# Kernel optimization log

Hardware: AMD Instinct MI355X
Metric: run time of the kernel (lower is better)

The kernel has to match this reference:

```python
import jax, jax.numpy as jnp
import numpy as np


def setup_inputs() -> dict:
    key = jax.random.key(0)
    ks = jax.random.split(key, 6)
    B, S, D_IN, D_OUT, E, R = 4, 2048, 4096, 4096, 8, 16
    x = jax.random.normal(ks[0], (B, S, D_IN), dtype=jnp.float32)
    probs = jax.random.uniform(ks[1], (B, E), dtype=jnp.float32)
    router_probs = probs / jnp.sum(probs, axis=-1, keepdims=True)
    weight = jax.random.normal(ks[2], (D_OUT, D_IN), dtype=jnp.float32) * 0.02
    bias = jax.random.normal(ks[3], (D_OUT,), dtype=jnp.float32) * 0.02
    lora_A = jax.random.normal(ks[4], (E, R, D_IN), dtype=jnp.float32) * 0.02
    lora_B = jax.random.normal(ks[5], (E, D_OUT, R), dtype=jnp.float32) * 0.02
    return {"x": x, "router_probs": router_probs, "weight": weight,
            "bias": bias, "lora_A": lora_A, "lora_B": lora_B}


def reference(x, router_probs, weight, bias, lora_A, lora_B):
    scaling = 2.0
    # base linear: [b,s,i] @ [o,i]^T + bias
    base_out = jnp.einsum('bsi,oi->bso', x, weight) + bias
    # low-rank per-expert projection: [b,s,e,r] (small: r=16)
    mid = jnp.einsum('bsi,eri->bser', x, lora_A)
    # weight by router probs (per batch, per expert) before up-projection
    mid_w = mid * router_probs[:, None, :, None]
    # sum over experts fused into the up-projection contraction
    delta = jnp.einsum('bser,eor->bso', mid_w, lora_B) * scaling
    return base_out + delta
```

## Files before the change

### kernel.cpp

```cpp
#include <hip/hip_runtime.h>


typedef _Float16 half8 __attribute__((ext_vector_type(8)));
typedef _Float16 half4 __attribute__((ext_vector_type(4)));
typedef float    f32x4 __attribute__((ext_vector_type(4)));

#define M_TOT 8192
#define N_TOT 4096
#define K_IN  4096
#define KA    4224
#define NT    132

__device__ __forceinline__ void cvt_store4(_Float16* p, float4 f) {
  half4 h;
  h[0] = (_Float16)f.x; h[1] = (_Float16)f.y;
  h[2] = (_Float16)f.z; h[3] = (_Float16)f.w;
  *(half4*)p = h;
}

template <int LOG2C, int DCOLS>
__global__ __launch_bounds__(256) void convert_f32_f16_t(
    const float* __restrict__ src, _Float16* __restrict__ dst, int total8) {
  for (int i = blockIdx.x * 256 + threadIdx.x; i < total8;
       i += gridDim.x * 256) {
    int base = i << 3;
    int r = base >> LOG2C;
    int c = base & ((1 << LOG2C) - 1);
    const float4* s = (const float4*)(src + (size_t)base);
    float4 f0 = s[0], f1 = s[1];
    half8 h;
    h[0]=(_Float16)f0.x; h[1]=(_Float16)f0.y; h[2]=(_Float16)f0.z; h[3]=(_Float16)f0.w;
    h[4]=(_Float16)f1.x; h[5]=(_Float16)f1.y; h[6]=(_Float16)f1.z; h[7]=(_Float16)f1.w;
    *(half8*)(dst + (size_t)r * DCOLS + c) = h;
  }
}

__global__ __launch_bounds__(256) void wtail_gather_f16(
    const float* __restrict__ loraB, _Float16* __restrict__ Wa) {
  int idx = blockIdx.x * 256 + threadIdx.x;
  int n = idx >> 7, j = idx & 127;
  int e = j >> 4, r = j & 15;
  Wa[(size_t)n * KA + K_IN + j] =
      (_Float16)loraB[((size_t)e * N_TOT + n) * 16 + r];
}

__global__ __launch_bounds__(256) void lorabf_gather_f32(
    const float* __restrict__ loraB, float* __restrict__ lorabf) {
  int idx = blockIdx.x * 256 + threadIdx.x;
  int n = idx >> 7, j = idx & 127;
  int e = j >> 4, r = j & 15;
  lorabf[(size_t)n * 128 + j] = loraB[((size_t)e * N_TOT + n) * 16 + r];
}

__global__ __launch_bounds__(256) void mid2_kernel(
    _Float16* __restrict__ Xa, const _Float16* __restrict__ lAh,
    const float* __restrict__ router) {
  __shared__ _Float16 As[32 * 64];
  __shared__ _Float16 Bs[128 * 64];
  int tid = threadIdx.x, lane = tid & 63, w = tid >> 6;
  int m0 = blockIdx.x * 32;
  int b = m0 >> 11;
  f32x4 acc[2][2] = {};

  for (int ks = 0; ks < 64; ++ks) {
    int kb = ks * 128;
    {
      const char* s = (const char*)Xa +
          (size_t)(m0 + w * 8 + (lane >> 3)) * (KA * 2) + kb + (lane & 7) * 16;
      __builtin_amdgcn_global_load_lds(
          (const __attribute__((address_space(1))) void*)s,
          (__attribute__((address_space(3))) void*)((char*)As + w * 1024), 16, 0, 0);
    }
#pragma unroll
    for (int i = 0; i < 4; ++i) {
      const char* s = (const char*)lAh +
          (size_t)((w * 4 + i) * 8 + (lane >> 3)) * (4096 * 2) + kb + (lane & 7) * 16;
      __builtin_amdgcn_global_load_lds(
          (const __attribute__((address_space(1))) void*)s,
          (__attribute__((address_space(3))) void*)((char*)Bs + (w * 4 + i) * 1024), 16, 0, 0);
    }
    __syncthreads();
#pragma unroll
    for (int kk = 0; kk < 2; ++kk) {
      half8 a[2], bf[2];
#pragma unroll
      for (int mi = 0; mi < 2; ++mi)
        a[mi] = *(const half8*)(As + (mi * 16 + (lane & 15)) * 64 + kk * 32 + (lane >> 4) * 8);
#pragma unroll
      for (int ni = 0; ni < 2; ++ni)
        bf[ni] = *(const half8*)(Bs + (w * 32 + ni * 16 + (lane & 15)) * 64 + kk * 32 + (lane >> 4) * 8);
#pragma unroll
      for (int mi = 0; mi < 2; ++mi)
#pragma unroll
        for (int ni = 0; ni < 2; ++ni)
          acc[mi][ni] = __builtin_amdgcn_mfma_f32_16x16x32_f16(a[mi], bf[ni], acc[mi][ni], 0, 0, 0);
    }
    __syncthreads();
  }

#pragma unroll
  for (int ni = 0; ni < 2; ++ni) {
    int j = w * 32 + ni * 16 + (lane & 15);
    int e = j >> 4;
    float sc = 2.0f * router[b * 8 + e];
#pragma unroll
    for (int mi = 0; mi < 2; ++mi) {
      f32x4 v = acc[mi][ni];
#pragma unroll
      for (int jj = 0; jj < 4; ++jj) {
        int m = m0 + mi * 16 + (lane >> 4) * 4 + jj;
        Xa[(size_t)m * KA + K_IN + j] = (_Float16)(v[jj] * sc);
      }
    }
  }
}

__global__ __launch_bounds__(256) void mid_kernel(
    const float* __restrict__ x, const float* __restrict__ loraA,
    const float* __restrict__ router, float* __restrict__ midw) {
  __shared__ _Float16 As[32 * 64];
  __shared__ _Float16 Bs[128 * 64];
  int tid = threadIdx.x, lane = tid & 63, w = tid >> 6;
  int m0 = blockIdx.x * 32;
  int b = m0 >> 11;
  f32x4 acc[2][2] = {};
  for (int ks = 0; ks < 64; ++ks) {
    int k0 = ks * 64;
#pragma unroll
    for (int it = 0; it < 2; ++it) {
      int idx = tid + it * 256;
      int r = idx >> 4, c4 = idx & 15;
      float4 f = *(const float4*)(x + (size_t)(m0 + r) * K_IN + k0 + c4 * 4);
      cvt_store4(As + r * 64 + c4 * 4, f);
    }
#pragma unroll
    for (int it = 0; it < 8; ++it) {
      int idx = tid + it * 256;
      int r = idx >> 4, c4 = idx & 15;
      float4 f = *(const float4*)(loraA + (size_t)r * K_IN + k0 + c4 * 4);
      cvt_store4(Bs + r * 64 + c4 * 4, f);
    }
    __syncthreads();
#pragma unroll
    for (int kk = 0; kk < 2; ++kk) {
      half8 a[2], bf[2];
#pragma unroll
      for (int mi = 0; mi < 2; ++mi)
        a[mi] = *(const half8*)(As + (mi * 16 + (lane & 15)) * 64 + kk * 32 + (lane >> 4) * 8);
#pragma unroll
      for (int ni = 0; ni < 2; ++ni)
        bf[ni] = *(const half8*)(Bs + (w * 32 + ni * 16 + (lane & 15)) * 64 + kk * 32 + (lane >> 4) * 8);
#pragma unroll
      for (int mi = 0; mi < 2; ++mi)
#pragma unroll
        for (int ni = 0; ni < 2; ++ni)
          acc[mi][ni] = __builtin_amdgcn_mfma_f32_16x16x32_f16(a[mi], bf[ni], acc[mi][ni], 0, 0, 0);
    }
    __syncthreads();
  }
#pragma unroll
  for (int ni = 0; ni < 2; ++ni) {
    int j = w * 32 + ni * 16 + (lane & 15);
    int e = j >> 4;
    float sc = 2.0f * router[b * 8 + e];
#pragma unroll
    for (int mi = 0; mi < 2; ++mi) {
      f32x4 v = acc[mi][ni];
#pragma unroll
      for (int jj = 0; jj < 4; ++jj) {
        int m = m0 + mi * 16 + (lane >> 4) * 4 + jj;
        midw[(size_t)m * 128 + j] = v[jj] * sc;
      }
    }
  }
}

#define BAR    __builtin_amdgcn_s_barrier()
#define SCHED0 __builtin_amdgcn_sched_barrier(0)
#define PRIO1  __builtin_amdgcn_s_setprio(1)
#define PRIO0  __builtin_amdgcn_s_setprio(0)
#define LGKM0  do { asm volatile("s_waitcnt lgkmcnt(0)" ::: "memory"); \
                    __builtin_amdgcn_sched_barrier(0); } while (0)
#define VMW8   asm volatile("s_waitcnt vmcnt(8)" ::: "memory")
#define VMW4   asm volatile("s_waitcnt vmcnt(4)" ::: "memory")
#define VMW0   asm volatile("s_waitcnt vmcnt(0)" ::: "memory")
#define GLOAD(src, dst) __builtin_amdgcn_global_load_lds( \
    (const __attribute__((address_space(1))) void*)(src), \
    (__attribute__((address_space(3))) void*)(dst), 16, 0, 0)

#define READS(SL) do { \
  _Pragma("unroll") for (int mi = 0; mi < 8; ++mi) \
    aF[mi] = *(const half8*)(LDS + (SL) * 16384 + \
                             (wm + mi * 16 + ln15) * 64 + rslot); \
  _Pragma("unroll") for (int ni = 0; ni < 4; ++ni) \
    bF[ni] = *(const half8*)(LDS + 65536 + (SL) * 16384 + \
                             (wn + ni * 16 + ln15) * 64 + rslot); \
  } while (0)

#define STAGE4(TT, SL) do { \
  const char* sA_ = XpC + (size_t)(TT) * 64; \
  const char* sB_ = WpC + (size_t)(TT) * 64; \
  GLOAD(sA_ + goff0, LDS + (SL) * 16384 + l0); \
  GLOAD(sA_ + goff1, LDS + (SL) * 16384 + l1); \
  GLOAD(sB_ + goff0, LDS + 65536 + (SL) * 16384 + l0); \
  GLOAD(sB_ + goff1, LDS + 65536 + (SL) * 16384 + l1); \
  } while (0)

#define MFMA32 do { \
  PRIO1; \
  _Pragma("unroll") for (int mi = 0; mi < 8; ++mi) \
    _Pragma("unroll") for (int ni = 0; ni < 4; ++ni) \
      acc[mi][ni] = __builtin_amdgcn_mfma_f32_16x16x32_f16( \
          aF[mi], bF[ni], acc[mi][ni], 0, 0, 0); \
  PRIO0; \
  } while (0)

#define TILE_FULL(SL) do { \
  READS(SL); \
  STAGE4(t4 + (SL) + 3, ((SL) + 3) & 3); \
  LGKM0; MFMA32; VMW8; BAR; SCHED0; \
  } while (0)

__global__ __launch_bounds__(512, 2) void gemm256(
    const _Float16* __restrict__ Xa, const _Float16* __restrict__ Wa,
    const float* __restrict__ bias, float* __restrict__ out) {
  __shared__ __align__(16) char LDS[131072];

  int tid = threadIdx.x, lane = tid & 63, w = tid >> 6;
  int ln15 = lane & 15, ln4 = lane >> 4;
  int wm = (w >> 2) * 128, wn = (w & 3) * 64;

  int bid = blockIdx.x;
  int xcd = bid & 7, idx = bid >> 3;
  int mt = (xcd & 3) * 8 + (idx & 7);
  int nt = (xcd >> 2) * 8 + (idx >> 3);
  int m0 = mt << 8, n0 = nt << 8;

  const char* XpC = (const char*)Xa + (size_t)m0 * (KA * 2);
  const char* WpC = (const char*)Wa + (size_t)n0 * (KA * 2);

  int i0 = tid, i1 = tid + 512;
  int goff0 = (i0 >> 2) * (KA * 2) + (((i0 & 3) ^ ((i0 >> 3) & 3)) * 16);
  int goff1 = (i1 >> 2) * (KA * 2) + (((i1 & 3) ^ ((i1 >> 3) & 3)) * 16);
  int l0 = i0 * 16, l1 = i1 * 16;

  int rslot = ((ln4 ^ ((lane >> 1) & 3)) * 16);

  f32x4 acc[8][4] = {};
  half8 aF[8], bF[4];

  STAGE4(0, 0); STAGE4(1, 1); STAGE4(2, 2);
  VMW8; BAR; SCHED0;

#pragma unroll 1
  for (int t4 = 0; t4 < NT - 4; t4 += 4) {
    TILE_FULL(0); TILE_FULL(1); TILE_FULL(2); TILE_FULL(3);
  }

  { READS(0); STAGE4(131, 3); LGKM0; MFMA32; VMW8; BAR; SCHED0; }
  { READS(1); LGKM0; MFMA32; VMW4; BAR; SCHED0; }
  { READS(2); LGKM0; MFMA32; VMW0; BAR; SCHED0; }
  { READS(3); LGKM0; MFMA32; }

#pragma unroll
  for (int ni = 0; ni < 4; ++ni) {
    int n = n0 + wn + ni * 16 + ln15;
    float bz = bias[n];
#pragma unroll
    for (int mi = 0; mi < 8; ++mi) {
      f32x4 v = acc[mi][ni];
      int mb = m0 + wm + mi * 16 + ln4 * 4;
#pragma unroll
      for (int jj = 0; jj < 4; ++jj)
        out[(size_t)(mb + jj) * N_TOT + n] = v[jj] + bz;
    }
  }
}

__global__ __launch_bounds__(256) void gemm_fallback(
    const float* __restrict__ x, const float* __restrict__ wgt,
    const float* __restrict__ midw, const float* __restrict__ lorabf,
    const float* __restrict__ bias, float* __restrict__ out) {
  __shared__ _Float16 As[128 * 64];
  __shared__ _Float16 Bs[128 * 64];
  int tid = threadIdx.x, lane = tid & 63, w = tid >> 6;
  int mt = blockIdx.x & 63, nt = blockIdx.x >> 6;
  int m0 = mt << 7, n0 = nt << 7;
  int wm = (w >> 1) * 64, wn = (w & 1) * 64;
  f32x4 acc[4][4] = {};
  for (int ks = 0; ks < 66; ++ks) {
    int k0 = ks * 64;
    const float *asrc, *bsrc; size_t astr, bstr; int ac, bc;
    if (ks < 64) { asrc = x;    astr = K_IN; ac = k0;        bsrc = wgt;    bstr = K_IN; bc = k0; }
    else         { asrc = midw; astr = 128;  ac = k0 - K_IN; bsrc = lorabf; bstr = 128;  bc = k0 - K_IN; }
#pragma unroll
    for (int it = 0; it < 8; ++it) {
      int idx = tid + it * 256;
      int r = idx >> 4, c4 = idx & 15;
      float4 fa = *(const float4*)(asrc + (size_t)(m0 + r) * astr + ac + c4 * 4);
      cvt_store4(As + r * 64 + c4 * 4, fa);
      float4 fb = *(const float4*)(bsrc + (size_t)(n0 + r) * bstr + bc + c4 * 4);
      cvt_store4(Bs + r * 64 + c4 * 4, fb);
    }
    __syncthreads();
#pragma unroll
    for (int kk = 0; kk < 2; ++kk) {
      half8 a[4], bf[4];
#pragma unroll
      for (int mi = 0; mi < 4; ++mi)
        a[mi] = *(const half8*)(As + (wm + mi * 16 + (lane & 15)) * 64 + kk * 32 + (lane >> 4) * 8);
#pragma unroll
      for (int ni = 0; ni < 4; ++ni)
        bf[ni] = *(const half8*)(Bs + (wn + ni * 16 + (lane & 15)) * 64 + kk * 32 + (lane >> 4) * 8);
#pragma unroll
      for (int mi = 0; mi < 4; ++mi)
#pragma unroll
        for (int ni = 0; ni < 4; ++ni)
          acc[mi][ni] = __builtin_amdgcn_mfma_f32_16x16x32_f16(a[mi], bf[ni], acc[mi][ni], 0, 0, 0);
    }
    __syncthreads();
  }
#pragma unroll
  for (int ni = 0; ni < 4; ++ni) {
    int n = n0 + wn + ni * 16 + (lane & 15);
    float bz = bias[n];
#pragma unroll
    for (int mi = 0; mi < 4; ++mi) {
      f32x4 v = acc[mi][ni];
      int mbase = m0 + wm + mi * 16 + (lane >> 4) * 4;
#pragma unroll
      for (int jj = 0; jj < 4; ++jj)
        out[(size_t)(mbase + jj) * N_TOT + n] = v[jj] + bz;
    }
  }
}

extern "C" void kernel_launch(void* const* d_in, const int* in_sizes, int n_in,
                              void* d_out, int out_size, void* d_ws, size_t ws_size,
                              hipStream_t stream) {
  const float* x      = (const float*)d_in[0];
  const float* router = (const float*)d_in[1];
  const float* wgt    = (const float*)d_in[2];
  const float* bias   = (const float*)d_in[3];
  const float* loraA  = (const float*)d_in[4];
  const float* loraB  = (const float*)d_in[5];
  float* out = (float*)d_out;
  char* ws = (char*)d_ws;

  const size_t XAUG_B = (size_t)M_TOT * KA * 2;
  const size_t WAUG_B = (size_t)N_TOT * KA * 2;
  const size_t LAH_B  = (size_t)128 * K_IN * 2;
  const size_t MIDW_B = (size_t)M_TOT * 128 * 4;
  bool fast = ws_size >= XAUG_B + WAUG_B + LAH_B;

  if (fast) {
    _Float16* Xa  = (_Float16*)ws;
    _Float16* Wa  = (_Float16*)(ws + XAUG_B);
    _Float16* lAh = (_Float16*)(ws + XAUG_B + WAUG_B);
    convert_f32_f16_t<12, KA><<<2048, 256, 0, stream>>>(x,   Xa, M_TOT * K_IN / 8);
    convert_f32_f16_t<12, KA><<<2048, 256, 0, stream>>>(wgt, Wa, N_TOT * K_IN / 8);
    convert_f32_f16_t<12, 4096><<<256, 256, 0, stream>>>(loraA, lAh, 128 * K_IN / 8);
    wtail_gather_f16<<<2048, 256, 0, stream>>>(loraB, Wa);
    mid2_kernel<<<256, 256, 0, stream>>>(Xa, lAh, router);
    gemm256<<<512, 512, 0, stream>>>(Xa, Wa, bias, out);
  } else {
    float* midw   = (float*)ws;
    float* lorabf = (float*)(ws + MIDW_B);
    lorabf_gather_f32<<<2048, 256, 0, stream>>>(loraB, lorabf);
    mid_kernel<<<256, 256, 0, stream>>>(x, loraA, router, midw);
    gemm_fallback<<<2048, 256, 0, stream>>>(x, wgt, midw, lorabf, bias, out);
  }
}
```

Before: 377.0 us.

## Restructure GEMM main loop into two-tile barrier groups with ping-pong fragments

Replaces the per-tile 4-slot pipeline, which issued one barrier and one vmcnt wait per K-tile, with a schedule that stages two tiles at a time and synchronises once per pair. Alternating even/odd register fragment sets let the LDS reads of one tile overlap the MFMAs of the previous one, since the explicit lgkmcnt waits and sched barriers are gone. The cost is a shallower prefetch: vmcnt(0) waits for all outstanding loads, and two extra fragment sets raise register pressure. Occupancy could drop under the launch bound of 512 threads with 2 blocks per CU.

```diff
diff --git a/kernel.cpp b/kernel.cpp
--- a/kernel.cpp
+++ b/kernel.cpp
@@ -179,22 +179,18 @@
 #define SCHED0 __builtin_amdgcn_sched_barrier(0)
 #define PRIO1  __builtin_amdgcn_s_setprio(1)
 #define PRIO0  __builtin_amdgcn_s_setprio(0)
-#define LGKM0  do { asm volatile("s_waitcnt lgkmcnt(0)" ::: "memory"); \
-                    __builtin_amdgcn_sched_barrier(0); } while (0)
-#define VMW8   asm volatile("s_waitcnt vmcnt(8)" ::: "memory")
-#define VMW4   asm volatile("s_waitcnt vmcnt(4)" ::: "memory")
 #define VMW0   asm volatile("s_waitcnt vmcnt(0)" ::: "memory")
 #define GLOAD(src, dst) __builtin_amdgcn_global_load_lds( \
     (const __attribute__((address_space(1))) void*)(src), \
     (__attribute__((address_space(3))) void*)(dst), 16, 0, 0)
 
-#define READS(SL) do { \
+#define READS(AF, BF, SL) do { \
+  _Pragma("unroll") for (int ni = 0; ni < 4; ++ni) \
+    BF[ni] = *(const half8*)(LDS + 65536 + (SL) * 16384 + \
+                             (wn + ni * 16 + ln15) * 64 + rslot); \
   _Pragma("unroll") for (int mi = 0; mi < 8; ++mi) \
-    aF[mi] = *(const half8*)(LDS + (SL) * 16384 + \
+    AF[mi] = *(const half8*)(LDS + (SL) * 16384 + \
                              (wm + mi * 16 + ln15) * 64 + rslot); \
-  _Pragma("unroll") for (int ni = 0; ni < 4; ++ni) \
-    bF[ni] = *(const half8*)(LDS + 65536 + (SL) * 16384 + \
-                             (wn + ni * 16 + ln15) * 64 + rslot); \
   } while (0)
 
 #define STAGE4(TT, SL) do { \
@@ -206,20 +202,16 @@
   GLOAD(sB_ + goff1, LDS + 65536 + (SL) * 16384 + l1); \
   } while (0)
 
-#define MFMA32 do { \
+#define MFMA32(AF, BF) do { \
   PRIO1; \
   _Pragma("unroll") for (int mi = 0; mi < 8; ++mi) \
     _Pragma("unroll") for (int ni = 0; ni < 4; ++ni) \
       acc[mi][ni] = __builtin_amdgcn_mfma_f32_16x16x32_f16( \
-          aF[mi], bF[ni], acc[mi][ni], 0, 0, 0); \
+          AF[mi], BF[ni], acc[mi][ni], 0, 0, 0); \
   PRIO0; \
   } while (0)
 
-#define TILE_FULL(SL) do { \
-  READS(SL); \
-  STAGE4(t4 + (SL) + 3, ((SL) + 3) & 3); \
-  LGKM0; MFMA32; VMW8; BAR; SCHED0; \
-  } while (0)
+#define TILE_NB(AF, BF, SL) do { READS(AF, BF, SL); MFMA32(AF, BF); } while (0)
 
 __global__ __launch_bounds__(512, 2) void gemm256(
     const _Float16* __restrict__ Xa, const _Float16* __restrict__ Wa,
@@ -247,20 +239,21 @@
   int rslot = ((ln4 ^ ((lane >> 1) & 3)) * 16);
 
   f32x4 acc[8][4] = {};
-  half8 aF[8], bF[4];
-
-  STAGE4(0, 0); STAGE4(1, 1); STAGE4(2, 2);
-  VMW8; BAR; SCHED0;
+  half8 aE[8], bE[4], aO[8], bO[4];
+
+  STAGE4(0, 0); STAGE4(1, 1);
 
 #pragma unroll 1
-  for (int t4 = 0; t4 < NT - 4; t4 += 4) {
-    TILE_FULL(0); TILE_FULL(1); TILE_FULL(2); TILE_FULL(3);
-  }
-
-  { READS(0); STAGE4(131, 3); LGKM0; MFMA32; VMW8; BAR; SCHED0; }
-  { READS(1); LGKM0; MFMA32; VMW4; BAR; SCHED0; }
-  { READS(2); LGKM0; MFMA32; VMW0; BAR; SCHED0; }
-  { READS(3); LGKM0; MFMA32; }
+  for (int t4 = 0; t4 < NT; t4 += 4) {
+    VMW0; BAR; SCHED0;
+    STAGE4(t4 + 2, 2); STAGE4(t4 + 3, 3);
+    TILE_NB(aE, bE, 0);
+    TILE_NB(aO, bO, 1);
+    VMW0; BAR; SCHED0;
+    if (t4 + 4 < NT) { STAGE4(t4 + 4, 0); STAGE4(t4 + 5, 1); }
+    TILE_NB(aE, bE, 2);
+    TILE_NB(aO, bO, 3);
+  }
 
 #pragma unroll
   for (int ni = 0; ni < 4; ++ni) {
```

Result: no change. 379.2 us (+0.6%).

## Shrink GEMM block tile to 128x256 with 3-stage LDS pipeline

Applied to the files above, without the earlier changes.

The main GEMM moves from a 256x256 block tile with 8 waves and a 4-stage LDS ring to a 128x256 block tile with 4 waves and a 3-stage ring. Each wave still computes a 128x64 sub-tile, and all waves share the A rows. Using 72KB of LDS lets two independent blocks fit per CU, so barriers no longer stall all 8 waves at once. The explicit lgkmcnt wait is removed, leaving LDS-read synchronisation to the compiler. The cost is less data reuse per block, so more global and L2 traffic for B and A, and a shallower prefetch depth.

```diff
diff --git a/kernel.cpp b/kernel.cpp
--- a/kernel.cpp
+++ b/kernel.cpp
@@ -179,31 +179,30 @@
 #define SCHED0 __builtin_amdgcn_sched_barrier(0)
 #define PRIO1  __builtin_amdgcn_s_setprio(1)
 #define PRIO0  __builtin_amdgcn_s_setprio(0)
-#define LGKM0  do { asm volatile("s_waitcnt lgkmcnt(0)" ::: "memory"); \
-                    __builtin_amdgcn_sched_barrier(0); } while (0)
-#define VMW8   asm volatile("s_waitcnt vmcnt(8)" ::: "memory")
-#define VMW4   asm volatile("s_waitcnt vmcnt(4)" ::: "memory")
+#define VMW6   asm volatile("s_waitcnt vmcnt(6)" ::: "memory")
 #define VMW0   asm volatile("s_waitcnt vmcnt(0)" ::: "memory")
 #define GLOAD(src, dst) __builtin_amdgcn_global_load_lds( \
     (const __attribute__((address_space(1))) void*)(src), \
     (__attribute__((address_space(3))) void*)(dst), 16, 0, 0)
 
 #define READS(SL) do { \
+  _Pragma("unroll") for (int ni = 0; ni < 4; ++ni) \
+    bF[ni] = *(const half8*)(LDS + 24576 + (SL) * 16384 + \
+                             (wn + ni * 16 + ln15) * 64 + rslot); \
   _Pragma("unroll") for (int mi = 0; mi < 8; ++mi) \
-    aF[mi] = *(const half8*)(LDS + (SL) * 16384 + \
-                             (wm + mi * 16 + ln15) * 64 + rslot); \
-  _Pragma("unroll") for (int ni = 0; ni < 4; ++ni) \
-    bF[ni] = *(const half8*)(LDS + 65536 + (SL) * 16384 + \
-                             (wn + ni * 16 + ln15) * 64 + rslot); \
+    aF[mi] = *(const half8*)(LDS + (SL) * 16384 / 2 + \
+                             (mi * 16 + ln15) * 64 + rslot); \
   } while (0)
 
-#define STAGE4(TT, SL) do { \
+#define STAGE6(TT, SL) do { \
   const char* sA_ = XpC + (size_t)(TT) * 64; \
   const char* sB_ = WpC + (size_t)(TT) * 64; \
-  GLOAD(sA_ + goff0, LDS + (SL) * 16384 + l0); \
-  GLOAD(sA_ + goff1, LDS + (SL) * 16384 + l1); \
-  GLOAD(sB_ + goff0, LDS + 65536 + (SL) * 16384 + l0); \
-  GLOAD(sB_ + goff1, LDS + 65536 + (SL) * 16384 + l1); \
+  GLOAD(sA_ + goffA[0], LDS + (SL) * 8192 + ldsA[0]); \
+  GLOAD(sA_ + goffA[1], LDS + (SL) * 8192 + ldsA[1]); \
+  GLOAD(sB_ + goffB[0], LDS + 24576 + (SL) * 16384 + ldsB[0]); \
+  GLOAD(sB_ + goffB[1], LDS + 24576 + (SL) * 16384 + ldsB[1]); \
+  GLOAD(sB_ + goffB[2], LDS + 24576 + (SL) * 16384 + ldsB[2]); \
+  GLOAD(sB_ + goffB[3], LDS + 24576 + (SL) * 16384 + ldsB[3]); \
   } while (0)
 
 #define MFMA32 do { \
@@ -215,52 +214,55 @@
   PRIO0; \
   } while (0)
 
-#define TILE_FULL(SL) do { \
-  READS(SL); \
-  STAGE4(t4 + (SL) + 3, ((SL) + 3) & 3); \
-  LGKM0; MFMA32; VMW8; BAR; SCHED0; \
-  } while (0)
-
-__global__ __launch_bounds__(512, 2) void gemm256(
+__global__ __launch_bounds__(256, 2) void gemm_main(
     const _Float16* __restrict__ Xa, const _Float16* __restrict__ Wa,
     const float* __restrict__ bias, float* __restrict__ out) {
-  __shared__ __align__(16) char LDS[131072];
+  __shared__ __align__(16) char LDS[73728];
 
   int tid = threadIdx.x, lane = tid & 63, w = tid >> 6;
   int ln15 = lane & 15, ln4 = lane >> 4;
-  int wm = (w >> 2) * 128, wn = (w & 3) * 64;
+  int wn = w * 64;
 
   int bid = blockIdx.x;
   int xcd = bid & 7, idx = bid >> 3;
-  int mt = (xcd & 3) * 8 + (idx & 7);
-  int nt = (xcd >> 2) * 8 + (idx >> 3);
-  int m0 = mt << 8, n0 = nt << 8;
+  int mt = (xcd & 3) * 16 + (idx & 15);
+  int nt = (xcd >> 2) * 8 + (idx >> 4);
+  int m0 = mt << 7, n0 = nt << 8;
 
   const char* XpC = (const char*)Xa + (size_t)m0 * (KA * 2);
   const char* WpC = (const char*)Wa + (size_t)n0 * (KA * 2);
 
-  int i0 = tid, i1 = tid + 512;
-  int goff0 = (i0 >> 2) * (KA * 2) + (((i0 & 3) ^ ((i0 >> 3) & 3)) * 16);
-  int goff1 = (i1 >> 2) * (KA * 2) + (((i1 & 3) ^ ((i1 >> 3) & 3)) * 16);
-  int l0 = i0 * 16, l1 = i1 * 16;
+  int goffA[2], ldsA[2], goffB[4], ldsB[4];
+#pragma unroll
+  for (int j = 0; j < 2; ++j) {
+    int i0 = j * 256 + tid;
+    goffA[j] = (i0 >> 2) * (KA * 2) + (((i0 & 3) ^ ((i0 >> 3) & 3)) * 16);
+    ldsA[j] = i0 * 16;
+  }
+#pragma unroll
+  for (int j = 0; j < 4; ++j) {
+    int i0 = j * 256 + tid;
+    goffB[j] = (i0 >> 2) * (KA * 2) + (((i0 & 3) ^ ((i0 >> 3) & 3)) * 16);
+    ldsB[j] = i0 * 16;
+  }
 
   int rslot = ((ln4 ^ ((lane >> 1) & 3)) * 16);
 
   f32x4 acc[8][4] = {};
   half8 aF[8], bF[4];
 
-  STAGE4(0, 0); STAGE4(1, 1); STAGE4(2, 2);
-  VMW8; BAR; SCHED0;
+  STAGE6(0, 0); STAGE6(1, 1);
+  VMW6; BAR; SCHED0;
 
 #pragma unroll 1
-  for (int t4 = 0; t4 < NT - 4; t4 += 4) {
-    TILE_FULL(0); TILE_FULL(1); TILE_FULL(2); TILE_FULL(3);
-  }
-
-  { READS(0); STAGE4(131, 3); LGKM0; MFMA32; VMW8; BAR; SCHED0; }
-  { READS(1); LGKM0; MFMA32; VMW4; BAR; SCHED0; }
-  { READS(2); LGKM0; MFMA32; VMW0; BAR; SCHED0; }
-  { READS(3); LGKM0; MFMA32; }
+  for (int t3 = 0; t3 < 129; t3 += 3) {
+    { READS(0); STAGE6(t3 + 2, 2); MFMA32; VMW6; BAR; SCHED0; }
+    { READS(1); STAGE6(t3 + 3, 0); MFMA32; VMW6; BAR; SCHED0; }
+    { READS(2); STAGE6(t3 + 4, 1); MFMA32; VMW6; BAR; SCHED0; }
+  }
+  { READS(0); STAGE6(131, 2); MFMA32; VMW6; BAR; SCHED0; }
+  { READS(1); MFMA32; VMW0; BAR; SCHED0; }
+  { READS(2); MFMA32; }
 
 #pragma unroll
   for (int ni = 0; ni < 4; ++ni) {
@@ -269,7 +271,7 @@
 #pragma unroll
     for (int mi = 0; mi < 8; ++mi) {
       f32x4 v = acc[mi][ni];
-      int mb = m0 + wm + mi * 16 + ln4 * 4;
+      int mb = m0 + mi * 16 + ln4 * 4;
 #pragma unroll
       for (int jj = 0; jj < 4; ++jj)
         out[(size_t)(mb + jj) * N_TOT + n] = v[jj] + bz;
@@ -362,7 +364,7 @@
     convert_f32_f16_t<12, 4096><<<256, 256, 0, stream>>>(loraA, lAh, 128 * K_IN / 8);
     wtail_gather_f16<<<2048, 256, 0, stream>>>(loraB, Wa);
     mid2_kernel<<<256, 256, 0, stream>>>(Xa, lAh, router);
-    gemm256<<<512, 512, 0, stream>>>(Xa, Wa, bias, out);
+    gemm_main<<<1024, 256, 0, stream>>>(Xa, Wa, bias, out);
   } else {
     float* midw   = (float*)ws;
     float* lorabf = (float*)(ws + MIDW_B);
```

Result: slower. 394.2 us (+4.6%).

## Interleave LDS reads with MFMA groups in main GEMM and swizzle mid2 LDS

Applied to the files above, without the earlier changes.

In the main GEMM loop, the per-tile LDS fragment reads are now interleaved with MFMA groups using sched_group_barrier. The global-to-LDS staging is issued first and the setprio toggles are dropped. The aim is to overlap LDS read latency with matrix math instead of waiting on all reads before computing. Separately, the mid2 low-rank kernel gains an XOR swizzle of the LDS layout to avoid bank conflicts. Removing the full lgkmcnt wait relies on the compiler inserting correct waits, and the scheduling hints may not be honored as intended.

```diff
diff --git a/kernel.cpp b/kernel.cpp
--- a/kernel.cpp
+++ b/kernel.cpp
@@ -62,33 +62,37 @@
   int b = m0 >> 11;
   f32x4 acc[2][2] = {};
 
+  int scol = ((lane & 7) ^ (lane >> 3)) * 16;
+  int ln15 = lane & 15, ln4 = lane >> 4;
+
   for (int ks = 0; ks < 64; ++ks) {
     int kb = ks * 128;
     {
       const char* s = (const char*)Xa +
-          (size_t)(m0 + w * 8 + (lane >> 3)) * (KA * 2) + kb + (lane & 7) * 16;
+          (size_t)(m0 + w * 8 + (lane >> 3)) * (KA * 2) + kb + scol;
       __builtin_amdgcn_global_load_lds(
           (const __attribute__((address_space(1))) void*)s,
-          (__attribute__((address_space(3))) void*)((char*)As + w * 1024), 16, 0, 0);
+          (__attribute__((address_space(3))) void*)((char*)As + w * 1024 + lane * 16), 16, 0, 0);
     }
 #pragma unroll
     for (int i = 0; i < 4; ++i) {
       const char* s = (const char*)lAh +
-          (size_t)((w * 4 + i) * 8 + (lane >> 3)) * (4096 * 2) + kb + (lane & 7) * 16;
+          (size_t)((w * 4 + i) * 8 + (lane >> 3)) * (4096 * 2) + kb + scol;
       __builtin_amdgcn_global_load_lds(
           (const __attribute__((address_space(1))) void*)s,
-          (__attribute__((address_space(3))) void*)((char*)Bs + (w * 4 + i) * 1024), 16, 0, 0);
+          (__attribute__((address_space(3))) void*)((char*)Bs + (w * 4 + i) * 1024 + lane * 16), 16, 0, 0);
     }
     __syncthreads();
 #pragma unroll
     for (int kk = 0; kk < 2; ++kk) {
+      int rs = (((kk * 4 + ln4) ^ (ln15 & 7)) << 4);
       half8 a[2], bf[2];
 #pragma unroll
       for (int mi = 0; mi < 2; ++mi)
-        a[mi] = *(const half8*)(As + (mi * 16 + (lane & 15)) * 64 + kk * 32 + (lane >> 4) * 8);
+        a[mi] = *(const half8*)((const char*)As + (mi * 16 + ln15) * 128 + rs);
 #pragma unroll
       for (int ni = 0; ni < 2; ++ni)
-        bf[ni] = *(const half8*)(Bs + (w * 32 + ni * 16 + (lane & 15)) * 64 + kk * 32 + (lane >> 4) * 8);
+        bf[ni] = *(const half8*)((const char*)Bs + (w * 32 + ni * 16 + ln15) * 128 + rs);
 #pragma unroll
       for (int mi = 0; mi < 2; ++mi)
 #pragma unroll
@@ -100,7 +104,7 @@
 
 #pragma unroll
   for (int ni = 0; ni < 2; ++ni) {
-    int j = w * 32 + ni * 16 + (lane & 15);
+    int j = w * 32 + ni * 16 + ln15;
     int e = j >> 4;
     float sc = 2.0f * router[b * 8 + e];
 #pragma unroll
@@ -108,7 +112,7 @@
       f32x4 v = acc[mi][ni];
 #pragma unroll
       for (int jj = 0; jj < 4; ++jj) {
-        int m = m0 + mi * 16 + (lane >> 4) * 4 + jj;
+        int m = m0 + mi * 16 + ln4 * 4 + jj;
         Xa[(size_t)m * KA + K_IN + j] = (_Float16)(v[jj] * sc);
       }
     }
@@ -177,24 +181,39 @@
 
 #define BAR    __builtin_amdgcn_s_barrier()
 #define SCHED0 __builtin_amdgcn_sched_barrier(0)
-#define PRIO1  __builtin_amdgcn_s_setprio(1)
-#define PRIO0  __builtin_amdgcn_s_setprio(0)
 #define LGKM0  do { asm volatile("s_waitcnt lgkmcnt(0)" ::: "memory"); \
                     __builtin_amdgcn_sched_barrier(0); } while (0)
 #define VMW8   asm volatile("s_waitcnt vmcnt(8)" ::: "memory")
 #define VMW4   asm volatile("s_waitcnt vmcnt(4)" ::: "memory")
 #define VMW0   asm volatile("s_waitcnt vmcnt(0)" ::: "memory")
+#define SGB(m, n) __builtin_amdgcn_sched_group_barrier((m), (n), 0)
 #define GLOAD(src, dst) __builtin_amdgcn_global_load_lds( \
     (const __attribute__((address_space(1))) void*)(src), \
     (__attribute__((address_space(3))) void*)(dst), 16, 0, 0)
 
-#define READS(SL) do { \
-  _Pragma("unroll") for (int mi = 0; mi < 8; ++mi) \
-    aF[mi] = *(const half8*)(LDS + (SL) * 16384 + \
-                             (wm + mi * 16 + ln15) * 64 + rslot); \
+#define READ_B4(SL) do { \
   _Pragma("unroll") for (int ni = 0; ni < 4; ++ni) \
     bF[ni] = *(const half8*)(LDS + 65536 + (SL) * 16384 + \
                              (wn + ni * 16 + ln15) * 64 + rslot); \
+  } while (0)
+
+#define READ_A1(mi, SL) \
+  aF[mi] = *(const half8*)(LDS + (SL) * 16384 + \
+                           (wm + (mi) * 16 + ln15) * 64 + rslot)
+
+#define MFMA_G(mi) do { \
+  _Pragma("unroll") for (int ni = 0; ni < 4; ++ni) \
+    acc[mi][ni] = __builtin_amdgcn_mfma_f32_16x16x32_f16( \
+        aF[mi], bF[ni], acc[mi][ni], 0, 0, 0); \
+  } while (0)
+
+#define MFMA32 do { \
+  _Pragma("unroll") for (int mi = 0; mi < 8; ++mi) MFMA_G(mi); \
+  } while (0)
+
+#define READS_ALL(SL) do { \
+  READ_B4(SL); \
+  _Pragma("unroll") for (int mi = 0; mi < 8; ++mi) READ_A1(mi, SL); \
   } while (0)
 
 #define STAGE4(TT, SL) do { \
@@ -206,19 +225,28 @@
   GLOAD(sB_ + goff1, LDS + 65536 + (SL) * 16384 + l1); \
   } while (0)
 
-#define MFMA32 do { \
-  PRIO1; \
-  _Pragma("unroll") for (int mi = 0; mi < 8; ++mi) \
-    _Pragma("unroll") for (int ni = 0; ni < 4; ++ni) \
-      acc[mi][ni] = __builtin_amdgcn_mfma_f32_16x16x32_f16( \
-          aF[mi], bF[ni], acc[mi][ni], 0, 0, 0); \
-  PRIO0; \
-  } while (0)
-
 #define TILE_FULL(SL) do { \
-  READS(SL); \
   STAGE4(t4 + (SL) + 3, ((SL) + 3) & 3); \
-  LGKM0; MFMA32; VMW8; BAR; SCHED0; \
+  READ_B4(SL); \
+  READ_A1(0, SL); \
+  READ_A1(1, SL); MFMA_G(0); \
+  READ_A1(2, SL); MFMA_G(1); \
+  READ_A1(3, SL); MFMA_G(2); \
+  READ_A1(4, SL); MFMA_G(3); \
+  READ_A1(5, SL); MFMA_G(4); \
+  READ_A1(6, SL); MFMA_G(5); \
+  READ_A1(7, SL); MFMA_G(6); \
+  MFMA_G(7); \
+  SGB(0x20, 4); SGB(0x100, 5); \
+  SGB(0x8, 4); SGB(0x100, 1); \
+  SGB(0x8, 4); SGB(0x100, 1); \
+  SGB(0x8, 4); SGB(0x100, 1); \
+  SGB(0x8, 4); SGB(0x100, 1); \
+  SGB(0x8, 4); SGB(0x100, 1); \
+  SGB(0x8, 4); SGB(0x100, 1); \
+  SGB(0x8, 4); SGB(0x100, 1); \
+  SGB(0x8, 4); \
+  VMW8; BAR; \
   } while (0)
 
 __global__ __launch_bounds__(512, 2) void gemm256(
@@ -257,10 +285,10 @@
     TILE_FULL(0); TILE_FULL(1); TILE_FULL(2); TILE_FULL(3);
   }
 
-  { READS(0); STAGE4(131, 3); LGKM0; MFMA32; VMW8; BAR; SCHED0; }
-  { READS(1); LGKM0; MFMA32; VMW4; BAR; SCHED0; }
-  { READS(2); LGKM0; MFMA32; VMW0; BAR; SCHED0; }
-  { READS(3); LGKM0; MFMA32; }
+  { READS_ALL(0); STAGE4(131, 3); LGKM0; MFMA32; VMW8; BAR; SCHED0; }
+  { READS_ALL(1); LGKM0; MFMA32; VMW4; BAR; SCHED0; }
+  { READS_ALL(2); LGKM0; MFMA32; VMW0; BAR; SCHED0; }
+  { READS_ALL(3); LGKM0; MFMA32; }
 
 #pragma unroll
   for (int ni = 0; ni < 4; ++ni) {
```

Result: no change. 374.7 us (-0.6%).
